# Kernel optimization log

Hardware: AMD Instinct MI355X
Metric: run time of the kernel (lower is better)

## Reference

```python
import jax, jax.numpy as jnp
import numpy as np
import math

B, C, N, M = 4, 512, 4096, 4096
DA = C // 4
BN_EPS = 1e-5

def setup_inputs() -> dict:
    key = jax.random.key(0)
    ks = jax.random.split(key, 10)
    s = 0.02
    return {
        "x": jax.random.normal(ks[0], (B, C, N), jnp.float32),
        "y": jax.random.normal(ks[1], (B, C, M), jnp.float32),
        # q_conv.weight is tied to k_conv.weight -> single shared [da, C] (no bias)
        "w_qk": jax.random.normal(ks[2], (DA, C), jnp.float32) * s,
        "w_v": jax.random.normal(ks[3], (C, C), jnp.float32) * s,
        "b_v": jax.random.normal(ks[4], (C,), jnp.float32) * s,
        "w_t": jax.random.normal(ks[5], (C, C), jnp.float32) * s,
        "b_t": jax.random.normal(ks[6], (C,), jnp.float32) * s,
        # BatchNorm1d (eval mode: use running stats)
        "gamma": jnp.ones((C,), jnp.float32),
        "beta": jnp.zeros((C,), jnp.float32),
        "run_mean": jax.random.normal(ks[7], (C,), jnp.float32) * 0.1,
        "run_var": jax.random.uniform(ks[8], (C,), jnp.float32, 0.5, 1.5),
    }

def reference(x, y, w_qk, w_v, b_v, w_t, b_t, gamma, beta, run_mean, run_var):
    scale = 1.0 / math.sqrt(DA)
    # 1x1 conv projections (shared q/k weight)
    q = jnp.einsum("dc,bcn->bdn", w_qk, x)                      # [B, da, N]
    k = jnp.einsum("dc,bcm->bdm", w_qk, y)                      # [B, da, M]
    v = jnp.einsum("oc,bcm->bom", w_v, y) + b_v[None, :, None]  # [B, C, M]
    energy = jnp.einsum("bdn,bdm->bnm", q, k) * scale           # [B, N, M]
    attn = jax.nn.softmax(energy, axis=-1)                      # softmax over keys M
    x_s = jnp.einsum("bcm,bnm->bcn", v, attn)                   # [B, C, N]
    x_s = jnp.einsum("oc,bcn->bon", w_t, x_s) + b_t[None, :, None]
    # BatchNorm1d (eval) over channel dim + ReLU
    inv = gamma / jnp.sqrt(run_var + BN_EPS)
    x_s = x_s * inv[None, :, None] + (beta - run_mean * inv)[None, :, None]
    x_s = jax.nn.relu(x_s)
    return jnp.transpose(x_s, (0, 2, 1))                        # [B, N, C]
```

## Files before the change

kernel.cpp:

```cpp
#include <hip/hip_runtime.h>
#include <hip/hip_bf16.h>
#include <stdint.h>

typedef __bf16 bf16;
typedef __bf16 bf16x8 __attribute__((ext_vector_type(8)));
typedef __bf16 bf16x4 __attribute__((ext_vector_type(4)));
typedef float  f32x4  __attribute__((ext_vector_type(4)));

template<typename T> __device__ __forceinline__ bf16x8 load8(const T* p);
template<> __device__ __forceinline__ bf16x8 load8<bf16>(const bf16* p) {
    return *(const bf16x8*)p;
}
template<> __device__ __forceinline__ bf16x8 load8<float>(const float* p) {
    f32x4 a = ((const f32x4*)p)[0];
    f32x4 b = ((const f32x4*)p)[1];
    bf16x8 r;
    #pragma unroll
    for (int m = 0; m < 4; m++) { r[m] = (bf16)a[m]; r[m + 4] = (bf16)b[m]; }
    return r;
}


__device__ __forceinline__ void gld16(bf16* lds, const bf16* g) {
    __builtin_amdgcn_global_load_lds(
        (const __attribute__((address_space(1))) void*)g,
        (__attribute__((address_space(3))) void*)lds, 16, 0, 0);
}

template<int ROWS>
__device__ __forceinline__ void stage(bf16* lds, const bf16* g, int64_t ld, int t) {
    constexpr int NI = ROWS / 32;
    const int w = t >> 6, l = t & 63;
    #pragma unroll
    for (int it = 0; it < NI; it++) {
        const int cb  = (it * 4 + w) * 64;
        const int c   = cb + l;
        const int row = c >> 3, col8 = (c & 7) ^ (row & 7);
        gld16(lds + (int64_t)cb * 8, g + (int64_t)row * ld + col8 * 8);
    }
}

__device__ __forceinline__ bf16x8 frag(const bf16* lds, int row, int g8) {
    return *(const bf16x8*)&lds[(row << 6) + ((g8 ^ (row & 7)) << 3)];
}

template<int BN_>
__device__ __forceinline__ void core_nt(bf16* As, bf16* Bs,
    const bf16* __restrict__ Ab, const bf16* __restrict__ Bb,
    int64_t ldA, int64_t ldB, int kbeg, int kend, f32x4 (*acc)[BN_ / 32])
{
    const int t = threadIdx.x, lane = t & 63, w = t >> 6;
    const int wi = (w >> 1) * 64, wj = (w & 1) * (BN_ / 2);
    const int quad = lane >> 4, l15 = lane & 15;
    for (int k0 = kbeg; k0 < kend; k0 += 64) {
        stage<128>(As, Ab + k0, ldA, t);
        stage<BN_>(Bs, Bb + k0, ldB, t);
        __syncthreads();
        #pragma unroll
        for (int kk = 0; kk < 64; kk += 32) {
            bf16x8 af[4], bfr[BN_ / 32];
            #pragma unroll
            for (int ti = 0; ti < 4; ti++)
                af[ti] = frag(As, wi + ti * 16 + l15, (kk >> 3) + quad);
            #pragma unroll
            for (int tj = 0; tj < BN_ / 32; tj++)
                bfr[tj] = frag(Bs, wj + tj * 16 + l15, (kk >> 3) + quad);
            #pragma unroll
            for (int ti = 0; ti < 4; ti++)
                #pragma unroll
                for (int tj = 0; tj < BN_ / 32; tj++)
                    acc[ti][tj] = __builtin_amdgcn_mfma_f32_16x16x32_bf16(
                        af[ti], bfr[tj], acc[ti][tj], 0, 0, 0);
        }
        __syncthreads();
    }
}

__global__ __launch_bounds__(256) void k_gemm_plain(
    const bf16* __restrict__ A, const bf16* __restrict__ Bm, bf16* __restrict__ Cc,
    int64_t sAz, int64_t sBz, int64_t sCz, int ldA, int ldB, int ldC, int K)
{
    __shared__ bf16 As[128 * 64];
    __shared__ bf16 Bs[128 * 64];
    const int i0 = blockIdx.y * 128, j0 = blockIdx.x * 128;
    const bf16* Ab = A  + blockIdx.z * sAz + (int64_t)i0 * ldA;
    const bf16* Bb = Bm + blockIdx.z * sBz + (int64_t)j0 * ldB;
    f32x4 acc[4][4] = {};
    core_nt<128>(As, Bs, Ab, Bb, ldA, ldB, 0, K, acc);

    bf16* Cb = Cc + blockIdx.z * sCz;
    const int lane = threadIdx.x & 63, w = threadIdx.x >> 6;
    const int wi = (w >> 1) * 64, wj = (w & 1) * 64, quad = lane >> 4, l15 = lane & 15;
    #pragma unroll
    for (int ti = 0; ti < 4; ti++)
        #pragma unroll
        for (int tj = 0; tj < 4; tj++) {
            const int jg = j0 + wj + tj * 16 + l15;
            #pragma unroll
            for (int r = 0; r < 4; r++)
                Cb[(int64_t)(i0 + wi + ti * 16 + quad * 4 + r) * ldC + jg] = (bf16)acc[ti][tj][r];
        }
}

__global__ __launch_bounds__(256) void k_eng(
    const bf16* __restrict__ Q, const bf16* __restrict__ Kt,
    bf16* __restrict__ P, float* __restrict__ L,
    int64_t sQz, int64_t sKz, int64_t sPz, int64_t sLz, int ldQ, int ldK, int ldP, int Kd)
{
    __shared__ bf16 As[128 * 64];
    __shared__ bf16 Bs[128 * 64];
    const int i0 = blockIdx.y * 128, j0 = blockIdx.x * 128;
    const bf16* Ab = Q  + blockIdx.z * sQz + (int64_t)i0 * ldQ;
    const bf16* Bb = Kt + blockIdx.z * sKz + (int64_t)j0 * ldK;
    f32x4 acc[4][4] = {};
    core_nt<128>(As, Bs, Ab, Bb, ldQ, ldK, 0, Kd, acc);

    bf16*  Pb = P + blockIdx.z * sPz;
    float* Lb = L + blockIdx.z * sLz;
    const int lane = threadIdx.x & 63, w = threadIdx.x >> 6;
    const int wi = (w >> 1) * 64, wj = (w & 1) * 64, quad = lane >> 4, l15 = lane & 15;
    #pragma unroll
    for (int ti = 0; ti < 4; ti++) {
        #pragma unroll
        for (int r = 0; r < 4; r++) {
            const int ig = i0 + wi + ti * 16 + quad * 4 + r;
            float s = 0.f;
            #pragma unroll
            for (int tj = 0; tj < 4; tj++) {
                const float e = __expf(acc[ti][tj][r]);
                s += e;
                Pb[(int64_t)ig * ldP + j0 + wj + tj * 16 + l15] = (bf16)e;
            }
            #pragma unroll
            for (int m = 1; m < 16; m <<= 1) s += __shfl_xor(s, m, 64);
            if (l15 == 0) atomicAdd(&Lb[ig], s);
        }
    }
}

__global__ __launch_bounds__(256) void k_recip(float* __restrict__ L, int n) {
    const int i = blockIdx.x * 256 + threadIdx.x;
    if (i < n) L[i] = 1.f / L[i];
}

template<bool PART>
__global__ __launch_bounds__(256) void k_z(
    const bf16* __restrict__ P, const bf16* __restrict__ Y, void* __restrict__ Zout,
    const float* __restrict__ Linv,
    int64_t sPz, int64_t sYz, int64_t sZz, int64_t sLz, int K, int KS)
{
    __shared__ bf16 As[128 * 64];
    __shared__ bf16 Bs[128 * 64];
    const int z = blockIdx.z;
    const int bz = z / KS, ks = z - bz * KS;
    const int i0 = blockIdx.y * 128, j0 = blockIdx.x * 128;
    const bf16* Ab = P + bz * sPz + (int64_t)i0 * K;
    const bf16* Bb = Y + bz * sYz + (int64_t)j0 * K;
    f32x4 acc[4][4] = {};
    const int KR = K / KS;
    core_nt<128>(As, Bs, Ab, Bb, K, K, ks * KR, ks * KR + KR, acc);

    const int lane = threadIdx.x & 63, w = threadIdx.x >> 6;
    const int wi = (w >> 1) * 64, wj = (w & 1) * 64, quad = lane >> 4, l15 = lane & 15;
    #pragma unroll
    for (int ti = 0; ti < 4; ti++)
        #pragma unroll
        for (int tj = 0; tj < 4; tj++) {
            const int jg = j0 + wj + tj * 16 + l15;
            #pragma unroll
            for (int r = 0; r < 4; r++) {
                const int ig = i0 + wi + ti * 16 + quad * 4 + r;
                if constexpr (PART)
                    ((float*)Zout)[(int64_t)ks * sZz + (int64_t)ig * 512 + jg] = acc[ti][tj][r];
                else
                    ((bf16*)Zout)[(int64_t)bz * sZz + (int64_t)ig * 512 + jg] =
                        (bf16)(acc[ti][tj][r] * Linv[bz * sLz + ig]);
            }
        }
}

__global__ __launch_bounds__(256) void k_zred(const float* __restrict__ Zp,
    bf16* __restrict__ Z, const float* __restrict__ Linv, int64_t n, int64_t slice, int KS)
{
    const int64_t idx = ((int64_t)blockIdx.x * 256 + threadIdx.x) * 8;
    if (idx >= n) return;
    f32x4 a0 = {}, a1 = {};
    for (int s = 0; s < KS; s++) {
        const float* p = Zp + (int64_t)s * slice + idx;
        a0 += *(const f32x4*)p;
        a1 += *(const f32x4*)(p + 4);
    }
    const float sc = Linv[idx >> 9];
    bf16x8 o;
    #pragma unroll
    for (int m = 0; m < 4; m++) { o[m] = (bf16)(a0[m] * sc); o[m + 4] = (bf16)(a1[m] * sc); }
    *(bf16x8*)&Z[idx] = o;
}

__global__ __launch_bounds__(256) void k_out(const int* __restrict__ flag,
    const bf16* __restrict__ Z, const bf16* __restrict__ W, void* __restrict__ outB,
    int64_t sZz, int64_t row0, int64_t rowz,
    const float* __restrict__ bias2,
    const void* gma, const void* bta, const void* mean, const void* var)
{
    __shared__ bf16 As[128 * 64];
    __shared__ bf16 Bs[128 * 64];
    const int i0 = blockIdx.y * 128, j0 = blockIdx.x * 128;
    const bf16* Ab = Z + blockIdx.z * sZz + (int64_t)i0 * 512;
    const bf16* Bb = W + (int64_t)j0 * 512;
    f32x4 acc[4][4] = {};
    core_nt<128>(As, Bs, Ab, Bb, 512, 512, 0, 512, acc);

    const int f = *flag;
    const int lane = threadIdx.x & 63, w = threadIdx.x >> 6;
    const int wi = (w >> 1) * 64, wj = (w & 1) * 64, quad = lane >> 4, l15 = lane & 15;
    const int64_t rbase = row0 + (int64_t)blockIdx.z * rowz;
    #pragma unroll
    for (int ti = 0; ti < 4; ti++)
        #pragma unroll
        for (int tj = 0; tj < 4; tj++) {
            const int jg = j0 + wj + tj * 16 + l15;
            float g, be, mn, vr;
            if (f) {
                g  = ((const float*)gma)[jg];  be = ((const float*)bta)[jg];
                mn = ((const float*)mean)[jg]; vr = ((const float*)var)[jg];
            } else {
                g  = (float)((const bf16*)gma)[jg];  be = (float)((const bf16*)bta)[jg];
                mn = (float)((const bf16*)mean)[jg]; vr = (float)((const bf16*)var)[jg];
            }
            const float inv = g * rsqrtf(vr + 1e-5f);
            const float add = be - mn * inv;
            const float bj  = bias2[jg];
            #pragma unroll
            for (int r = 0; r < 4; r++) {
                const int ig = i0 + wi + ti * 16 + quad * 4 + r;
                float val = (acc[ti][tj][r] + bj) * inv + add;
                val = fmaxf(val, 0.f);
                if (f) ((float*)outB)[(rbase + ig) * 512 + jg] = val;
                else   ((bf16*)outB)[(rbase + ig) * 512 + jg] = (bf16)val;
            }
        }
}

template<typename TA>
__device__ __forceinline__ void proj_core(bf16 (*As)[72], bf16 (*Bs)[72],
    const TA* __restrict__ Ag, const bf16* __restrict__ Bg, int64_t ldA, f32x4 (*acc)[4])
{
    const int t = threadIdx.x, lane = t & 63, w = t >> 6;
    const int wi = (w >> 1) * 64, wj = (w & 1) * 64;
    const int quad = lane >> 4, l15 = lane & 15;
    for (int k0 = 0; k0 < 512; k0 += 64) {
        #pragma unroll
        for (int gi = 0; gi < 4; gi++) {
            const int c = t * 4 + gi, k = c >> 4, i8 = c & 15;
            bf16x8 v = load8<TA>(Ag + (int64_t)(k0 + k) * ldA + i8 * 8);
            #pragma unroll
            for (int m = 0; m < 8; m++) As[i8 * 8 + m][k] = v[m];
        }
        #pragma unroll
        for (int gi = 0; gi < 4; gi++) {
            const int c = t * 4 + gi, r = c >> 3, kg = c & 7;
            *(bf16x8*)&Bs[r][kg * 8] = *(const bf16x8*)(Bg + r * 512 + k0 + kg * 8);
        }
        __syncthreads();
        #pragma unroll
        for (int kk = 0; kk < 64; kk += 32) {
            bf16x8 af[4], bfr[4];
            #pragma unroll
            for (int ti = 0; ti < 4; ti++)
                af[ti] = *(const bf16x8*)&As[wi + ti * 16 + l15][kk + quad * 8];
            #pragma unroll
            for (int tj = 0; tj < 4; tj++)
                bfr[tj] = *(const bf16x8*)&Bs[wj + tj * 16 + l15][kk + quad * 8];
            #pragma unroll
            for (int ti = 0; ti < 4; ti++)
                #pragma unroll
                for (int tj = 0; tj < 4; tj++)
                    acc[ti][tj] = __builtin_amdgcn_mfma_f32_16x16x32_bf16(
                        af[ti], bfr[tj], acc[ti][tj], 0, 0, 0);
        }
        __syncthreads();
    }
}

__global__ __launch_bounds__(256) void k_proj(const int* __restrict__ flag,
    const void* __restrict__ X, int64_t sX, const bf16* __restrict__ wqk,
    bf16* __restrict__ Q, int64_t sQ, int ldX, float scale)
{
    __shared__ bf16 As[128][72];
    __shared__ bf16 Bs[128][72];
    const int i0 = blockIdx.y * 128;
    f32x4 acc[4][4] = {};
    if (*flag)
        proj_core<float>(As, Bs, (const float*)X + blockIdx.z * sX + i0, wqk, ldX, acc);
    else
        proj_core<bf16>(As, Bs, (const bf16*)X + blockIdx.z * sX + i0, wqk, ldX, acc);

    bf16* C = Q + blockIdx.z * sQ;
    const int lane = threadIdx.x & 63, w = threadIdx.x >> 6;
    const int wi = (w >> 1) * 64, wj = (w & 1) * 64, quad = lane >> 4, l15 = lane & 15;
    #pragma unroll
    for (int ti = 0; ti < 4; ti++)
        #pragma unroll
        for (int tj = 0; tj < 4; tj++) {
            const int jg = wj + tj * 16 + l15;
            #pragma unroll
            for (int r = 0; r < 4; r++) {
                const int ig = i0 + wi + ti * 16 + quad * 4 + r;
                C[(int64_t)ig * 128 + jg] = (bf16)(acc[ti][tj][r] * scale);
            }
        }
}

__global__ void k_detect(const void* gma, int* flag) {
    if (threadIdx.x == 0 && blockIdx.x == 0) {
        uint16_t h = ((const uint16_t*)gma)[0];
        *flag = (h == 0x3F80u) ? 0 : 1;
    }
}

__global__ __launch_bounds__(256) void k_cvt(const int* __restrict__ flag,
    const void* __restrict__ in, bf16* __restrict__ outp, int64_t n)
{
    const int64_t idx = ((int64_t)blockIdx.x * 256 + threadIdx.x) * 8;
    if (idx >= n) return;
    bf16x8 v = (*flag) ? load8<float>((const float*)in + idx)
                       : load8<bf16>((const bf16*)in + idx);
    *(bf16x8*)&outp[idx] = v;
}

__global__ __launch_bounds__(256) void k_tr(const int* __restrict__ flag,
    const void* __restrict__ in, bf16* __restrict__ outp, int R, int Cc)
{
    __shared__ float tile[64][65];
    const int r0 = blockIdx.y * 64, c0 = blockIdx.x * 64;
    const int t = threadIdx.x;
    const int rl = t >> 4, cl = (t & 15) * 4;
    const int f = *flag;
    #pragma unroll
    for (int p = 0; p < 4; p++) {
        const int r = rl + p * 16;
        if (f) {
            f32x4 v = *(const f32x4*)((const float*)in + (int64_t)(r0 + r) * Cc + c0 + cl);
            #pragma unroll
            for (int m = 0; m < 4; m++) tile[r][cl + m] = v[m];
        } else {
            const bf16* q = (const bf16*)in + (int64_t)(r0 + r) * Cc + c0 + cl;
            #pragma unroll
            for (int m = 0; m < 4; m++) tile[r][cl + m] = (float)q[m];
        }
    }
    __syncthreads();
    #pragma unroll
    for (int p = 0; p < 4; p++) {
        const int crow = rl + p * 16;
        bf16x4 o;
        #pragma unroll
        for (int m = 0; m < 4; m++) o[m] = (bf16)tile[cl + m][crow];
        *(bf16x4*)(outp + (int64_t)(c0 + crow) * R + r0 + cl) = o;
    }
}

__global__ __launch_bounds__(256) void k_bias2(const int* __restrict__ flag,
    const void* bv, const void* wt, const void* bt, float* __restrict__ bias2)
{
    const int o = blockIdx.x, t = threadIdx.x;
    const int f = *flag;
    float s = 0.f;
    for (int c = t; c < 512; c += 256) {
        float b, wv;
        if (f) { b = ((const float*)bv)[c]; wv = ((const float*)wt)[(int64_t)o * 512 + c]; }
        else   { b = (float)((const bf16*)bv)[c]; wv = (float)((const bf16*)wt)[(int64_t)o * 512 + c]; }
        s += b * wv;
    }
    #pragma unroll
    for (int off = 1; off < 64; off <<= 1) s += __shfl_xor(s, off, 64);
    __shared__ float red[4];
    if ((t & 63) == 0) red[t >> 6] = s;
    __syncthreads();
    if (t == 0) {
        float tot = red[0] + red[1] + red[2] + red[3];
        float btv = f ? ((const float*)bt)[o] : (float)((const bf16*)bt)[o];
        bias2[o] = tot + btv;
    }
}

extern "C" void kernel_launch(void* const* d_in, const int* in_sizes, int n_in,
                              void* d_out, int out_size, void* d_ws, size_t ws_size,
                              hipStream_t stream)
{
    constexpr int B = 4, C = 512, N = 4096, M = 4096, DA = 128;
    const float scale = 0.08838834764831845f;

    const void* x    = d_in[0];
    const void* y    = d_in[1];
    const void* w_qk = d_in[2];
    const void* w_v  = d_in[3];
    const void* b_v  = d_in[4];
    const void* w_t  = d_in[5];
    const void* b_t  = d_in[6];
    const void* gma  = d_in[7];
    const void* bta  = d_in[8];
    const void* rmean= d_in[9];
    const void* rvar = d_in[10];

    char* ws = (char*)d_ws;
    size_t off = 0;
    auto take = [&](size_t nbytes) { size_t p = off; off = (off + nbytes + 255) & ~(size_t)255; return p; };
    int*   flag  = (int*)  (ws + take(4));
    float* bias2 = (float*)(ws + take(512 * 4));
    bf16*  wqkb  = (bf16*) (ws + take((size_t)DA * C * 2));
    bf16*  wtb   = (bf16*) (ws + take((size_t)C * C * 2));
    bf16*  wvT   = (bf16*) (ws + take((size_t)C * C * 2));
    bf16*  W     = (bf16*) (ws + take((size_t)C * C * 2));
    bf16*  qT    = (bf16*) (ws + take((size_t)B * N * DA * 2));
    bf16*  kT    = (bf16*) (ws + take((size_t)B * M * DA * 2));
    bf16*  yb    = (bf16*) (ws + take((size_t)B * C * M * 2));
    if (off > ws_size) return;
    const size_t rem = ws_size - off;

    int bsz = 1, chunk = 0, KS = 1;
    if      (rem >= (size_t)4 * N * ((M + C) * 2 + 4)) { bsz = 4; chunk = N; }
    else if (rem >= (size_t)2 * N * ((M + C) * 2 + 4)) { bsz = 2; chunk = N; }
    else {
        const int candC[] = {4096, 2048, 4096, 1024, 2048, 512, 1024, 256, 512, 128, 256, 128};
        const int candK[] = {4,    4,    1,    4,    1,    4,   1,    4,   1,   4,   1,   1};
        for (int i = 0; i < 12; i++) {
            size_t need = (size_t)candC[i] * ((M + C) * 2 + 4)
                        + (candK[i] > 1 ? (size_t)candK[i] * candC[i] * C * 4 : 0);
            if (need <= rem) { chunk = candC[i]; KS = candK[i]; break; }
        }
        if (!chunk) return;
    }

    bf16*  P  = (bf16*) (ws + take((size_t)bsz * chunk * M * 2));
    bf16*  Z  = (bf16*) (ws + take((size_t)bsz * chunk * C * 2));
    float* L  = (float*)(ws + take((size_t)bsz * chunk * 4));
    float* Zp = nullptr;
    if (KS > 1) Zp = (float*)(ws + take((size_t)KS * chunk * C * 4));
    if (off > ws_size) return;

    dim3 blk(256);

    k_detect<<<1, 64, 0, stream>>>(gma, flag);
    k_cvt<<<dim3((DA * C) / 2048), blk, 0, stream>>>(flag, w_qk, wqkb, (int64_t)DA * C);
    k_cvt<<<dim3((C * C) / 2048), blk, 0, stream>>>(flag, w_t, wtb, (int64_t)C * C);
    k_cvt<<<dim3((unsigned)(((size_t)B * C * M) / 2048)), blk, 0, stream>>>(
        flag, y, yb, (int64_t)B * C * M);
    k_tr<<<dim3(C / 64, C / 64), blk, 0, stream>>>(flag, w_v, wvT, C, C);
    k_gemm_plain<<<dim3(C / 128, C / 128, 1), blk, 0, stream>>>(
        wtb, wvT, W, 0, 0, 0, C, C, C, C);
    k_bias2<<<C, blk, 0, stream>>>(flag, b_v, w_t, b_t, bias2);

    k_proj<<<dim3(1, N / 128, B), blk, 0, stream>>>(
        flag, x, (int64_t)C * N, wqkb, qT, (int64_t)N * DA, N, scale);
    k_proj<<<dim3(1, M / 128, B), blk, 0, stream>>>(
        flag, y, (int64_t)C * M, wqkb, kT, (int64_t)M * DA, M, 1.f);

    for (int b0 = 0; b0 < B; b0 += bsz) {
        for (int n0 = 0; n0 < N; n0 += chunk) {
            const int nrows = bsz * chunk;
            hipMemsetAsync(L, 0, (size_t)nrows * 4, stream);

            k_eng<<<dim3(M / 128, chunk / 128, bsz), blk, 0, stream>>>(
                qT + ((size_t)b0 * N + n0) * DA, kT + (size_t)b0 * M * DA, P, L,
                (int64_t)N * DA, (int64_t)M * DA, (int64_t)chunk * M, (int64_t)chunk,
                DA, DA, M, DA);

            k_recip<<<(nrows + 255) / 256, blk, 0, stream>>>(L, nrows);

            if (KS > 1) {
                k_z<true><<<dim3(C / 128, chunk / 128, bsz * KS), blk, 0, stream>>>(
                    P, yb + (size_t)b0 * C * M, Zp, L,
                    (int64_t)chunk * M, (int64_t)C * M, (int64_t)chunk * C, (int64_t)chunk,
                    M, KS);
                k_zred<<<dim3((unsigned)(((size_t)chunk * C) / 2048)), blk, 0, stream>>>(
                    Zp, Z, L, (int64_t)chunk * C, (int64_t)chunk * C, KS);
            } else {
                k_z<false><<<dim3(C / 128, chunk / 128, bsz), blk, 0, stream>>>(
                    P, yb + (size_t)b0 * C * M, Z, L,
                    (int64_t)chunk * M, (int64_t)C * M, (int64_t)chunk * C, (int64_t)chunk,
                    M, 1);
            }

            k_out<<<dim3(C / 128, chunk / 128, bsz), blk, 0, stream>>>(
                flag, Z, W, d_out, (int64_t)chunk * C, (int64_t)b0 * N + n0, (int64_t)N,
                bias2, gma, bta, rmean, rvar);
        }
    }

    (void)in_sizes; (void)n_in; (void)out_size;
}
```

Measured before the change: 357.0 us.

## Fuse y bf16 conversion into projection, inline reciprocal, add batched split-K

Drops the separate y-to-bf16 conversion kernel by having the key projection write the converted y tile as it loads it. Removes the k_recip launch by computing 1/L inline in the Z epilogue and the reduction. Generalises the split-K path to batch multiple batches at once and prefers bsz=4 with KS=2 when workspace allows, which doubles the Z GEMM grid at the cost of an fp32 partial buffer and an extra reduction pass.

```diff
diff --git a/kernel.cpp b/kernel.cpp
--- a/kernel.cpp
+++ b/kernel.cpp
@@ -138,15 +138,10 @@
     }
 }
 
-__global__ __launch_bounds__(256) void k_recip(float* __restrict__ L, int n) {
-    const int i = blockIdx.x * 256 + threadIdx.x;
-    if (i < n) L[i] = 1.f / L[i];
-}
-
 template<bool PART>
 __global__ __launch_bounds__(256) void k_z(
     const bf16* __restrict__ P, const bf16* __restrict__ Y, void* __restrict__ Zout,
-    const float* __restrict__ Linv,
+    const float* __restrict__ L,
     int64_t sPz, int64_t sYz, int64_t sZz, int64_t sLz, int K, int KS)
 {
     __shared__ bf16 As[128 * 64];
@@ -163,34 +158,41 @@
     const int lane = threadIdx.x & 63, w = threadIdx.x >> 6;
     const int wi = (w >> 1) * 64, wj = (w & 1) * 64, quad = lane >> 4, l15 = lane & 15;
     #pragma unroll
-    for (int ti = 0; ti < 4; ti++)
-        #pragma unroll
-        for (int tj = 0; tj < 4; tj++) {
-            const int jg = j0 + wj + tj * 16 + l15;
-            #pragma unroll
-            for (int r = 0; r < 4; r++) {
-                const int ig = i0 + wi + ti * 16 + quad * 4 + r;
+    for (int ti = 0; ti < 4; ti++) {
+        #pragma unroll
+        for (int r = 0; r < 4; r++) {
+            const int ig = i0 + wi + ti * 16 + quad * 4 + r;
+            float linv = 0.f;
+            if constexpr (!PART) linv = 1.f / L[bz * sLz + ig];
+            #pragma unroll
+            for (int tj = 0; tj < 4; tj++) {
+                const int jg = j0 + wj + tj * 16 + l15;
                 if constexpr (PART)
-                    ((float*)Zout)[(int64_t)ks * sZz + (int64_t)ig * 512 + jg] = acc[ti][tj][r];
+                    ((float*)Zout)[(int64_t)(bz * KS + ks) * sZz + (int64_t)ig * 512 + jg] =
+                        acc[ti][tj][r];
                 else
                     ((bf16*)Zout)[(int64_t)bz * sZz + (int64_t)ig * 512 + jg] =
-                        (bf16)(acc[ti][tj][r] * Linv[bz * sLz + ig]);
+                        (bf16)(acc[ti][tj][r] * linv);
             }
         }
+    }
 }
 
 __global__ __launch_bounds__(256) void k_zred(const float* __restrict__ Zp,
-    bf16* __restrict__ Z, const float* __restrict__ Linv, int64_t n, int64_t slice, int KS)
+    bf16* __restrict__ Z, const float* __restrict__ L,
+    int64_t n, int64_t slice, int KS)
 {
     const int64_t idx = ((int64_t)blockIdx.x * 256 + threadIdx.x) * 8;
     if (idx >= n) return;
+    const int64_t bz = idx / slice, rm = idx - bz * slice;
+    const float* base = Zp + (int64_t)bz * KS * slice + rm;
     f32x4 a0 = {}, a1 = {};
     for (int s = 0; s < KS; s++) {
-        const float* p = Zp + (int64_t)s * slice + idx;
+        const float* p = base + (int64_t)s * slice;
         a0 += *(const f32x4*)p;
         a1 += *(const f32x4*)(p + 4);
     }
-    const float sc = Linv[idx >> 9];
+    const float sc = 1.f / L[idx >> 9];
     bf16x8 o;
     #pragma unroll
     for (int m = 0; m < 4; m++) { o[m] = (bf16)(a0[m] * sc); o[m + 4] = (bf16)(a1[m] * sc); }
@@ -244,7 +246,8 @@
 
 template<typename TA>
 __device__ __forceinline__ void proj_core(bf16 (*As)[72], bf16 (*Bs)[72],
-    const TA* __restrict__ Ag, const bf16* __restrict__ Bg, int64_t ldA, f32x4 (*acc)[4])
+    const TA* __restrict__ Ag, const bf16* __restrict__ Bg, int64_t ldA,
+    bf16* __restrict__ yc, f32x4 (*acc)[4])
 {
     const int t = threadIdx.x, lane = t & 63, w = t >> 6;
     const int wi = (w >> 1) * 64, wj = (w & 1) * 64;
@@ -254,6 +257,7 @@
         for (int gi = 0; gi < 4; gi++) {
             const int c = t * 4 + gi, k = c >> 4, i8 = c & 15;
             bf16x8 v = load8<TA>(Ag + (int64_t)(k0 + k) * ldA + i8 * 8);
+            if (yc) *(bf16x8*)(yc + (int64_t)(k0 + k) * ldA + i8 * 8) = v;
             #pragma unroll
             for (int m = 0; m < 8; m++) As[i8 * 8 + m][k] = v[m];
         }
@@ -285,16 +289,18 @@
 
 __global__ __launch_bounds__(256) void k_proj(const int* __restrict__ flag,
     const void* __restrict__ X, int64_t sX, const bf16* __restrict__ wqk,
-    bf16* __restrict__ Q, int64_t sQ, int ldX, float scale)
+    bf16* __restrict__ Q, int64_t sQ, bf16* __restrict__ yc, int64_t sYc,
+    int ldX, float scale)
 {
     __shared__ bf16 As[128][72];
     __shared__ bf16 Bs[128][72];
     const int i0 = blockIdx.y * 128;
+    bf16* ycb = yc ? yc + blockIdx.z * sYc + i0 : nullptr;
     f32x4 acc[4][4] = {};
     if (*flag)
-        proj_core<float>(As, Bs, (const float*)X + blockIdx.z * sX + i0, wqk, ldX, acc);
+        proj_core<float>(As, Bs, (const float*)X + blockIdx.z * sX + i0, wqk, ldX, ycb, acc);
     else
-        proj_core<bf16>(As, Bs, (const bf16*)X + blockIdx.z * sX + i0, wqk, ldX, acc);
+        proj_core<bf16>(As, Bs, (const bf16*)X + blockIdx.z * sX + i0, wqk, ldX, ycb, acc);
 
     bf16* C = Q + blockIdx.z * sQ;
     const int lane = threadIdx.x & 63, w = threadIdx.x >> 6;
@@ -419,16 +425,21 @@
     if (off > ws_size) return;
     const size_t rem = ws_size - off;
 
-    int bsz = 1, chunk = 0, KS = 1;
-    if      (rem >= (size_t)4 * N * ((M + C) * 2 + 4)) { bsz = 4; chunk = N; }
-    else if (rem >= (size_t)2 * N * ((M + C) * 2 + 4)) { bsz = 2; chunk = N; }
+    auto fits = [&](int bs, int ch, int ks) {
+        size_t need = (size_t)bs * ch * (M + C) * 2 + (size_t)bs * ch * 4
+                    + (ks > 1 ? (size_t)bs * ks * ch * C * 4 : 0);
+        return need <= rem;
+    };
+
+    int bsz = 0, chunk = 0, KS = 1;
+    if      (fits(4, N, 2)) { bsz = 4; chunk = N; KS = 2; }
+    else if (fits(4, N, 1)) { bsz = 4; chunk = N; KS = 1; }
+    else if (fits(2, N, 1)) { bsz = 2; chunk = N; KS = 1; }
     else {
-        const int candC[] = {4096, 2048, 4096, 1024, 2048, 512, 1024, 256, 512, 128, 256, 128};
-        const int candK[] = {4,    4,    1,    4,    1,    4,   1,    4,   1,   4,   1,   1};
-        for (int i = 0; i < 12; i++) {
-            size_t need = (size_t)candC[i] * ((M + C) * 2 + 4)
-                        + (candK[i] > 1 ? (size_t)candK[i] * candC[i] * C * 4 : 0);
-            if (need <= rem) { chunk = candC[i]; KS = candK[i]; break; }
+        const int candC[] = {2048, 4096, 1024, 2048, 512, 1024, 256, 512, 128, 256, 128};
+        const int candK[] = {4,    1,    4,    1,    4,   1,    4,   1,   4,   1,   1};
+        for (int i = 0; i < 11; i++) {
+            if (fits(1, candC[i], candK[i])) { bsz = 1; chunk = candC[i]; KS = candK[i]; break; }
         }
         if (!chunk) return;
     }
@@ -437,7 +448,7 @@
     bf16*  Z  = (bf16*) (ws + take((size_t)bsz * chunk * C * 2));
     float* L  = (float*)(ws + take((size_t)bsz * chunk * 4));
     float* Zp = nullptr;
-    if (KS > 1) Zp = (float*)(ws + take((size_t)KS * chunk * C * 4));
+    if (KS > 1) Zp = (float*)(ws + take((size_t)bsz * KS * chunk * C * 4));
     if (off > ws_size) return;
 
     dim3 blk(256);
@@ -445,17 +456,15 @@
     k_detect<<<1, 64, 0, stream>>>(gma, flag);
     k_cvt<<<dim3((DA * C) / 2048), blk, 0, stream>>>(flag, w_qk, wqkb, (int64_t)DA * C);
     k_cvt<<<dim3((C * C) / 2048), blk, 0, stream>>>(flag, w_t, wtb, (int64_t)C * C);
-    k_cvt<<<dim3((unsigned)(((size_t)B * C * M) / 2048)), blk, 0, stream>>>(
-        flag, y, yb, (int64_t)B * C * M);
     k_tr<<<dim3(C / 64, C / 64), blk, 0, stream>>>(flag, w_v, wvT, C, C);
     k_gemm_plain<<<dim3(C / 128, C / 128, 1), blk, 0, stream>>>(
         wtb, wvT, W, 0, 0, 0, C, C, C, C);
     k_bias2<<<C, blk, 0, stream>>>(flag, b_v, w_t, b_t, bias2);
 
     k_proj<<<dim3(1, N / 128, B), blk, 0, stream>>>(
-        flag, x, (int64_t)C * N, wqkb, qT, (int64_t)N * DA, N, scale);
+        flag, x, (int64_t)C * N, wqkb, qT, (int64_t)N * DA, nullptr, 0, N, scale);
     k_proj<<<dim3(1, M / 128, B), blk, 0, stream>>>(
-        flag, y, (int64_t)C * M, wqkb, kT, (int64_t)M * DA, M, 1.f);
+        flag, y, (int64_t)C * M, wqkb, kT, (int64_t)M * DA, yb, (int64_t)C * M, M, 1.f);
 
     for (int b0 = 0; b0 < B; b0 += bsz) {
         for (int n0 = 0; n0 < N; n0 += chunk) {
@@ -466,16 +475,14 @@
                 qT + ((size_t)b0 * N + n0) * DA, kT + (size_t)b0 * M * DA, P, L,
                 (int64_t)N * DA, (int64_t)M * DA, (int64_t)chunk * M, (int64_t)chunk,
                 DA, DA, M, DA);
-
-            k_recip<<<(nrows + 255) / 256, blk, 0, stream>>>(L, nrows);
 
             if (KS > 1) {
                 k_z<true><<<dim3(C / 128, chunk / 128, bsz * KS), blk, 0, stream>>>(
                     P, yb + (size_t)b0 * C * M, Zp, L,
                     (int64_t)chunk * M, (int64_t)C * M, (int64_t)chunk * C, (int64_t)chunk,
                     M, KS);
-                k_zred<<<dim3((unsigned)(((size_t)chunk * C) / 2048)), blk, 0, stream>>>(
-                    Zp, Z, L, (int64_t)chunk * C, (int64_t)chunk * C, KS);
+                k_zred<<<dim3((unsigned)(((size_t)bsz * chunk * C) / 2048)), blk, 0, stream>>>(
+                    Zp, Z, L, (int64_t)bsz * chunk * C, (int64_t)chunk * C, KS);
             } else {
                 k_z<false><<<dim3(C / 128, chunk / 128, bsz), blk, 0, stream>>>(
                     P, yb + (size_t)b0 * C * M, Z, L,
```

Result: slower. 371.6 us (+4.1%).
